# Kernel tuning notes

Hardware: AMD Instinct MI355X
Metric: run time of the kernel (lower is better)

## Reference

```python
import jax, jax.numpy as jnp
import numpy as np

N = 50000      # nodes
E = 800000     # edges (before self loops)
IN = 128       # in_ch
HID = 128      # hid (conv1 concat output)
OUT = 128      # out_ch
H = 4          # heads in conv1
NEG_SLOPE = 0.2


def setup_inputs() -> dict:
    key = jax.random.key(0)
    ks = jax.random.split(key, 16)
    s = 0.05
    return {
        "x": jax.random.normal(ks[0], (N, IN), dtype=jnp.float32),
        "edge_index": jax.random.randint(ks[1], (2, E), 0, N, dtype=jnp.int64),
        # conv1 params (heads=4, per-head dim HID//H)
        "W1l": jax.random.normal(ks[2], (IN, HID), dtype=jnp.float32) * s,
        "b1l": jnp.zeros((HID,), jnp.float32),
        "W1r": jax.random.normal(ks[3], (IN, HID), dtype=jnp.float32) * s,
        "b1r": jnp.zeros((HID,), jnp.float32),
        "att1": jax.random.normal(ks[4], (H, HID // H), dtype=jnp.float32) * s,
        "bias1": jnp.zeros((HID,), jnp.float32),
        # conv2 params (heads=1)
        "W2l": jax.random.normal(ks[5], (HID, OUT), dtype=jnp.float32) * s,
        "b2l": jnp.zeros((OUT,), jnp.float32),
        "W2r": jax.random.normal(ks[6], (HID, OUT), dtype=jnp.float32) * s,
        "b2r": jnp.zeros((OUT,), jnp.float32),
        "att2": jax.random.normal(ks[7], (1, OUT), dtype=jnp.float32) * s,
        "bias2": jnp.zeros((OUT,), jnp.float32),
    }


def gatv2_conv(x, src, dst, Wl, bl, Wr, br, att, heads):
    """PyG GATv2Conv (share_weights=False, concat=True).
    message(j->i): e = LeakyReLU(x_l[j] + x_r[i]); logit = <e, att>;
    softmax over edges per destination i; out_i = sum alpha * x_l[j].
    """
    n = x.shape[0]
    c = Wl.shape[1] // heads
    xl = (x @ Wl + bl).reshape(n, heads, c)   # source transform
    xr = (x @ Wr + br).reshape(n, heads, c)   # destination transform
    e = jax.nn.leaky_relu(xl[src] + xr[dst], NEG_SLOPE)      # [E, H, C]
    logits = jnp.einsum("ehc,hc->eh", e, att)                 # [E, H]
    m = jax.lax.stop_gradient(
        jax.ops.segment_max(logits, dst, num_segments=n))     # [N, H]
    p = jnp.exp(logits - m[dst])                              # [E, H]
    denom = jax.ops.segment_sum(p, dst, num_segments=n)       # [N, H]
    alpha = p / denom[dst]                                    # [E, H]
    out = jax.ops.segment_sum(xl[src] * alpha[..., None], dst,
                              num_segments=n)                 # [N, H, C]
    return out.reshape(n, heads * c)


def reference(x, edge_index, W1l, b1l, W1r, b1r, att1, bias1,
              W2l, b2l, W2r, b2r, att2, bias2):
    n = x.shape[0]
    # PyG default add_self_loops=True
    loops = jnp.arange(n, dtype=edge_index.dtype)
    src = jnp.concatenate([edge_index[0], loops])
    dst = jnp.concatenate([edge_index[1], loops])
    h = gatv2_conv(x, src, dst, W1l, b1l, W1r, b1r, att1, H) + bias1
    h = jax.nn.relu(h)
    out = gatv2_conv(h, src, dst, W2l, b2l, W2r, b2r, att2, 1) + bias2
    return out
```

## Files before the change

kernel.cpp:

```cpp
#include <hip/hip_runtime.h>
#include <hip/hip_bf16.h>

#define NODES 50000
#define NEDGE 800000
#define CH 128
#define NEG_SLOPE 0.2f
#define SCAN_CHUNK 2048
#define NBLK ((NODES + SCAN_CHUNK - 1) / SCAN_CHUNK)
#define NINF -1.0e30f
#define LOG2E 1.44269504088896340736f
#define NSLICE 400
#define SSLICE (NEDGE / NSLICE)

typedef short short8 __attribute__((ext_vector_type(8)));
typedef float f32x4 __attribute__((ext_vector_type(4)));

__device__ __forceinline__ unsigned fbits(float f) {
    union { float f; unsigned u; } v; v.f = f; return v.u;
}
__device__ __forceinline__ float asf(unsigned u) {
    union { float f; unsigned u; } v; v.u = u; return v.f;
}
__device__ __forceinline__ unsigned short f2bf(float f) {
    unsigned u = fbits(f);
    unsigned r = u + 0x7fff + ((u >> 16) & 1);
    return (unsigned short)(r >> 16);
}
__device__ __forceinline__ float bf2f(unsigned short h) {
    return asf(((unsigned)h) << 16);
}
__device__ __forceinline__ float lrelu(float x) {
    return fmaxf(x, NEG_SLOPE * x);
}
__device__ __forceinline__ void bf8cvt(uint4 u, float* f) {
    f[0] = asf(u.x << 16); f[1] = asf(u.x & 0xFFFF0000u);
    f[2] = asf(u.y << 16); f[3] = asf(u.y & 0xFFFF0000u);
    f[4] = asf(u.z << 16); f[5] = asf(u.z & 0xFFFF0000u);
    f[6] = asf(u.w << 16); f[7] = asf(u.w & 0xFFFF0000u);
}
__device__ __forceinline__ int dset(int dst) {
    return (int)(((unsigned)dst * 8u) / 50000u);
}

__global__ __launch_bounds__(256) void detect_zero_kernel(const void* idx,
                                                          int* flag, int* cnt) {
    int t = blockIdx.x * 256 + (int)threadIdx.x;
    if (t < NODES) cnt[t] = 0;
    if (blockIdx.x == 0 && threadIdx.x < 64) {
        const int* w = (const int*)idx;
        int nz = (w[2 * threadIdx.x + 1] != 0) ? 1 : 0;
        unsigned long long b = __ballot(nz);
        if (threadIdx.x == 0) *flag = (b == 0ull) ? 1 : 0;
    }
}

__global__ __launch_bounds__(256) void hist_part_kernel(const void* idx,
                                                        const int* flag,
                                                        int* cnt) {
    int set = blockIdx.x & 7;
    int slice = blockIdx.x >> 3;
    int base = slice * SSLICE;
    int endE = base + SSLICE;
    int i64 = *flag;
    const int* w = (const int*)idx;
    for (int e = base + (int)threadIdx.x; e < endE; e += 256) {
        int dst = i64 ? w[2 * (NEDGE + e)] : w[NEDGE + e];
        if (dset(dst) == set) atomicAdd(&cnt[dst], 1);
    }
}

__global__ __launch_bounds__(256) void scan1_kernel(const int* __restrict__ cnt,
                                                    int* __restrict__ bsum) {
    int base = blockIdx.x * SCAN_CHUNK + (int)threadIdx.x * 8;
    int s = 0;
    #pragma unroll
    for (int k = 0; k < 8; ++k) {
        int i = base + k;
        s += (i < NODES) ? cnt[i] : 0;
    }
    #pragma unroll
    for (int m = 1; m < 64; m <<= 1) s += __shfl_xor(s, m);
    __shared__ int ws[4];
    if ((threadIdx.x & 63) == 0) ws[threadIdx.x >> 6] = s;
    __syncthreads();
    if (threadIdx.x == 0) bsum[blockIdx.x] = ws[0] + ws[1] + ws[2] + ws[3];
}

__global__ __launch_bounds__(256) void scan3_kernel(const int* __restrict__ cnt,
                                                    const int* __restrict__ bsum,
                                                    int* __restrict__ offs,
                                                    int* __restrict__ cursor) {
    int tid = (int)threadIdx.x;
    int bpre = 0;
    #pragma unroll
    for (int b = 0; b < NBLK; ++b) bpre += (b < (int)blockIdx.x) ? bsum[b] : 0;

    int base = blockIdx.x * SCAN_CHUNK + tid * 8;
    int v[8];
    int s = 0;
    #pragma unroll
    for (int k = 0; k < 8; ++k) {
        int i = base + k;
        v[k] = (i < NODES) ? cnt[i] : 0;
        s += v[k];
    }
    int lane = tid & 63;
    int incl = s;
    #pragma unroll
    for (int m = 1; m < 64; m <<= 1) {
        int t = __shfl_up(incl, m);
        if (lane >= m) incl += t;
    }
    __shared__ int wtot[4];
    if (lane == 63) wtot[tid >> 6] = incl;
    __syncthreads();
    int w = tid >> 6;
    int wbase = 0;
    #pragma unroll
    for (int k = 0; k < 4; ++k) wbase += (k < w) ? wtot[k] : 0;
    int excl = bpre + wbase + (incl - s);
    #pragma unroll
    for (int k = 0; k < 8; ++k) {
        int i = base + k;
        if (i < NODES) { offs[i] = excl; cursor[i] = excl; }
        excl += v[k];
    }
    if (blockIdx.x == 0 && tid == 0) offs[NODES] = NEDGE;
}

__global__ __launch_bounds__(256) void scatter_part_kernel(const void* idx,
                                                           const int* flag,
                                                           int* cursor,
                                                           int* __restrict__ srcs) {
    int set = blockIdx.x & 7;
    int slice = blockIdx.x >> 3;
    int base = slice * SSLICE;
    int endE = base + SSLICE;
    int i64 = *flag;
    const int* w = (const int*)idx;
    for (int e = base + (int)threadIdx.x; e < endE; e += 256) {
        int dst = i64 ? w[2 * (NEDGE + e)] : w[NEDGE + e];
        if (dset(dst) == set) {
            int src = i64 ? w[2 * e] : w[e];
            int pos = atomicAdd(&cursor[dst], 1);
            srcs[pos] = src;
        }
    }
}

__global__ __launch_bounds__(256) void wprep4_kernel(const float* __restrict__ W0,
                                                     const float* __restrict__ W1,
                                                     const float* __restrict__ W2,
                                                     const float* __restrict__ W3,
                                                     unsigned short* __restrict__ base) {
    int which = blockIdx.x >> 6;
    const float* W = (which == 0) ? W0 : (which == 1) ? W1 : (which == 2) ? W2 : W3;
    unsigned short* hiT = base + (size_t)which * 32768;
    unsigned short* loT = hiT + 16384;
    int i = (blockIdx.x & 63) * 256 + (int)threadIdx.x;
    int k = i >> 7, n = i & 127;
    float f = W[i];
    unsigned short h = f2bf(f);
    unsigned short l = f2bf(f - bf2f(h));
    hiT[n * CH + k] = h;
    loT[n * CH + k] = l;
}

#define GR 64
#define LDP 136

__global__ __launch_bounds__(256) void gemm_dual_mfma(
        const float* __restrict__ X,
        const unsigned short* __restrict__ whTl, const unsigned short* __restrict__ wlTl,
        const unsigned short* __restrict__ whTr, const unsigned short* __restrict__ wlTr,
        const float* __restrict__ bl, const float* __restrict__ br,
        unsigned short* __restrict__ Ylb, float* __restrict__ Yr, int nrows) {
    __shared__ unsigned short xh[GR][LDP];
    __shared__ unsigned short xlo[GR][LDP];

    int r0 = blockIdx.x * GR;
    int tid = (int)threadIdx.x;

    {
        int row = tid >> 2;
        int c0 = (tid & 3) * 32;
        const float* src = X + (size_t)(r0 + row) * CH + c0;
        bool valid = (r0 + row) < nrows;
        #pragma unroll
        for (int j = 0; j < 32; j += 4) {
            float4 v = valid ? *(const float4*)(src + j)
                             : make_float4(0.f, 0.f, 0.f, 0.f);
            unsigned ux = fbits(v.x), uy = fbits(v.y);
            unsigned uz = fbits(v.z), uw = fbits(v.w);
            unsigned hx = ux & 0xFFFF0000u, hy = uy & 0xFFFF0000u;
            unsigned hz = uz & 0xFFFF0000u, hw = uw & 0xFFFF0000u;
            uint2 hp;
            hp.x = (ux >> 16) | hy;
            hp.y = (uz >> 16) | hw;
            float lx = v.x - asf(hx), ly = v.y - asf(hy);
            float lz = v.z - asf(hz), lw = v.w - asf(hw);
            uint2 lp;
            lp.x = (fbits(lx) >> 16) | (fbits(ly) & 0xFFFF0000u);
            lp.y = (fbits(lz) >> 16) | (fbits(lw) & 0xFFFF0000u);
            *(uint2*)&xh[row][c0 + j]  = hp;
            *(uint2*)&xlo[row][c0 + j] = lp;
        }
    }
    __syncthreads();

    int wave = tid >> 6;
    int lane = tid & 63;
    int l15 = lane & 15, q = lane >> 4;

    f32x4 acc[4][4];
    #pragma unroll
    for (int mt = 0; mt < 4; ++mt)
        #pragma unroll
        for (int nt = 0; nt < 4; ++nt) acc[mt][nt] = (f32x4)0.f;

    const unsigned short* bhp[4];
    const unsigned short* blp_[4];
    int ncol[4];
    #pragma unroll
    for (int nt = 0; nt < 4; ++nt) {
        int n = (wave * 4 + nt) * 16 + l15;
        ncol[nt] = n;
        int nn = n & 127;
        bhp[nt]  = ((n < CH) ? whTl : whTr) + (size_t)nn * CH;
        blp_[nt] = ((n < CH) ? wlTl : wlTr) + (size_t)nn * CH;
    }

    for (int kt = 0; kt < 4; ++kt) {
        int kofs = kt * 32 + q * 8;
        short8 ah[4], al[4];
        #pragma unroll
        for (int mt = 0; mt < 4; ++mt) {
            ah[mt] = *(const short8*)&xh[mt * 16 + l15][kofs];
            al[mt] = *(const short8*)&xlo[mt * 16 + l15][kofs];
        }
        #pragma unroll
        for (int nt = 0; nt < 4; ++nt) {
            short8 bh8 = *(const short8*)(bhp[nt] + kofs);
            short8 bl8 = *(const short8*)(blp_[nt] + kofs);
            #pragma unroll
            for (int mt = 0; mt < 4; ++mt) {
                acc[mt][nt] = __builtin_amdgcn_mfma_f32_16x16x32_bf16(
                                  ah[mt], bh8, acc[mt][nt], 0, 0, 0);
                acc[mt][nt] = __builtin_amdgcn_mfma_f32_16x16x32_bf16(
                                  al[mt], bh8, acc[mt][nt], 0, 0, 0);
                acc[mt][nt] = __builtin_amdgcn_mfma_f32_16x16x32_bf16(
                                  ah[mt], bl8, acc[mt][nt], 0, 0, 0);
            }
        }
    }

    #pragma unroll
    for (int nt = 0; nt < 4; ++nt) {
        int n = ncol[nt];
        int nc = n & 127;
        if (n < CH) {
            float bv = bl[nc];
            #pragma unroll
            for (int mt = 0; mt < 4; ++mt)
                #pragma unroll
                for (int reg = 0; reg < 4; ++reg) {
                    int row = r0 + mt * 16 + q * 4 + reg;
                    if (row < nrows)
                        Ylb[(size_t)row * CH + nc] = f2bf(acc[mt][nt][reg] + bv);
                }
        } else {
            float bv = br[nc];
            #pragma unroll
            for (int mt = 0; mt < 4; ++mt)
                #pragma unroll
                for (int reg = 0; reg < 4; ++reg) {
                    int row = r0 + mt * 16 + q * 4 + reg;
                    if (row < nrows)
                        Yr[(size_t)row * CH + nc] = acc[mt][nt][reg] + bv;
                }
        }
    }
}

template <int HEADS, bool RELU>
__global__ __launch_bounds__(256) void node_pass(
        const unsigned short* __restrict__ xlb,
        const float* __restrict__ xr,
        const float* __restrict__ att,
        const float* __restrict__ bias,
        const int* __restrict__ offs, const int* __restrict__ srcs,
        float* __restrict__ out) {
    constexpr int GL = (CH / HEADS) / 8;
    int wave = (int)threadIdx.x >> 6;
    int i = blockIdx.x * 4 + wave;
    int lane = (int)threadIdx.x & 63;
    int g = lane >> 4;
    int l16 = lane & 15;
    int c0 = l16 * 8;

    float r[8], a[8], s[8];
    {
        const float4* xrp = (const float4*)(xr + (size_t)i * CH + c0);
        float4 r0 = xrp[0], r1 = xrp[1];
        r[0]=r0.x; r[1]=r0.y; r[2]=r0.z; r[3]=r0.w;
        r[4]=r1.x; r[5]=r1.y; r[6]=r1.z; r[7]=r1.w;
        const float4* atp = (const float4*)(att + c0);
        float4 a0 = atp[0], a1 = atp[1];
        a[0]=a0.x*LOG2E; a[1]=a0.y*LOG2E; a[2]=a0.z*LOG2E; a[3]=a0.w*LOG2E;
        a[4]=a1.x*LOG2E; a[5]=a1.y*LOG2E; a[6]=a1.z*LOG2E; a[7]=a1.w*LOG2E;
    }
    uint4 us = *(const uint4*)(xlb + (size_t)i * CH + c0);
    bf8cvt(us, s);

    float ts = 0.f;
    #pragma unroll
    for (int c = 0; c < 8; ++c) ts += lrelu(s[c] + r[c]) * a[c];
    #pragma unroll
    for (int msk = 1; msk < GL; msk <<= 1) ts += __shfl_xor(ts, msk);

    float m = (g == 0) ? ts : NINF;
    float d = (g == 0) ? 1.f : 0.f;
    float acc[8];
    #pragma unroll
    for (int c = 0; c < 8; ++c) acc[c] = (g == 0) ? s[c] : 0.f;

    int beg = offs[i], end = offs[i + 1];
    int deg = end - beg;
    int iters = (deg + 3) >> 2;
    if (iters > 0) {
        int last = end - 1;
        int e = beg + g;
        int si = srcs[min(e, last)];
        uint4 u = *(const uint4*)(xlb + (size_t)si * CH + c0);

        for (int it = 0; it < iters; ++it, e += 4) {
            bool valid = e < end;
            int sn = srcs[min(e + 4, last)];
            uint4 un = *(const uint4*)(xlb + (size_t)sn * CH + c0);

            float f[8];
            bf8cvt(u, f);
            float t = 0.f;
            #pragma unroll
            for (int c = 0; c < 8; ++c) t += lrelu(f[c] + r[c]) * a[c];
            #pragma unroll
            for (int msk = 1; msk < GL; msk <<= 1) t += __shfl_xor(t, msk);
            t = valid ? t : NINF;

            float nm = fmaxf(m, t);
            float sc = exp2f(m - nm);
            float p  = valid ? exp2f(t - nm) : 0.f;
            d = d * sc + p;
            #pragma unroll
            for (int c = 0; c < 8; ++c) acc[c] = acc[c] * sc + p * f[c];
            m = nm;
            u = un;
        }
    }

    #pragma unroll
    for (int msk = 16; msk <= 32; msk <<= 1) {
        float mo  = __shfl_xor(m, msk);
        float dof = __shfl_xor(d, msk);
        float nm = fmaxf(m, mo);
        float s0 = exp2f(m - nm), s1 = exp2f(mo - nm);
        d = d * s0 + dof * s1;
        #pragma unroll
        for (int c = 0; c < 8; ++c) {
            float ao = __shfl_xor(acc[c], msk);
            acc[c] = acc[c] * s0 + ao * s1;
        }
        m = nm;
    }

    if (g == 0) {
        float inv = 1.0f / d;
        const float4* bp = (const float4*)(bias + c0);
        float4 b0 = bp[0], b1 = bp[1];
        float bb[8] = {b0.x, b0.y, b0.z, b0.w, b1.x, b1.y, b1.z, b1.w};
        float o[8];
        #pragma unroll
        for (int c = 0; c < 8; ++c) {
            o[c] = acc[c] * inv + bb[c];
            if (RELU) o[c] = fmaxf(o[c], 0.f);
        }
        float4 w0 = make_float4(o[0], o[1], o[2], o[3]);
        float4 w1 = make_float4(o[4], o[5], o[6], o[7]);
        float4* op = (float4*)(out + (size_t)i * CH + c0);
        op[0] = w0; op[1] = w1;
    }
}

extern "C" void kernel_launch(void* const* d_in, const int* in_sizes, int n_in,
                              void* d_out, int out_size, void* d_ws, size_t ws_size,
                              hipStream_t stream) {
    const float* x     = (const float*)d_in[0];
    const void*  eidx  = d_in[1];
    const float* W1l   = (const float*)d_in[2];
    const float* b1l   = (const float*)d_in[3];
    const float* W1r   = (const float*)d_in[4];
    const float* b1r   = (const float*)d_in[5];
    const float* att1  = (const float*)d_in[6];
    const float* bias1 = (const float*)d_in[7];
    const float* W2l   = (const float*)d_in[8];
    const float* b2l   = (const float*)d_in[9];
    const float* W2r   = (const float*)d_in[10];
    const float* b2r   = (const float*)d_in[11];
    const float* att2  = (const float*)d_in[12];
    const float* bias2 = (const float*)d_in[13];
    float* out = (float*)d_out;

    unsigned short* xlb = (unsigned short*)d_ws;
    float* xr = (float*)(xlb + (size_t)NODES * CH);
    float* hb = xr + (size_t)NODES * CH;
    int* offs   = (int*)(hb + (size_t)NODES * CH);
    int* cnt    = offs + (NODES + 1);
    int* cursor = cnt + NODES;
    int* srcs   = cursor + NODES;
    int* flag   = srcs + NEDGE;
    int* bsum   = flag + 1;

    unsigned short* wbuf = (unsigned short*)cnt;
    unsigned short* w1lh = wbuf;              unsigned short* w1ll = wbuf + 16384;
    unsigned short* w1rh = wbuf + 32768;      unsigned short* w1rl = wbuf + 49152;
    unsigned short* w2lh = wbuf + 65536;      unsigned short* w2ll = wbuf + 81920;
    unsigned short* w2rh = wbuf + 98304;      unsigned short* w2rl = wbuf + 114688;

    const int GG = (NODES + GR - 1) / GR;
    const int ZB = (NODES + 255) / 256;
    const int PG = NSLICE * 8;

    detect_zero_kernel<<<ZB, 256, 0, stream>>>(eidx, flag, cnt);
    hist_part_kernel<<<PG, 256, 0, stream>>>(eidx, flag, cnt);
    scan1_kernel<<<NBLK, 256, 0, stream>>>(cnt, bsum);
    scan3_kernel<<<NBLK, 256, 0, stream>>>(cnt, bsum, offs, cursor);
    scatter_part_kernel<<<PG, 256, 0, stream>>>(eidx, flag, cursor, srcs);

    wprep4_kernel<<<256, 256, 0, stream>>>(W1l, W1r, W2l, W2r, wbuf);

    gemm_dual_mfma<<<GG, 256, 0, stream>>>(x, w1lh, w1ll, w1rh, w1rl,
                                           b1l, b1r, xlb, xr, NODES);
    node_pass<4, true><<<(NODES + 3) / 4, 256, 0, stream>>>(xlb, xr, att1, bias1,
                                                            offs, srcs, hb);

    gemm_dual_mfma<<<GG, 256, 0, stream>>>(hb, w2lh, w2ll, w2rh, w2rl,
                                           b2l, b2r, xlb, xr, NODES);
    node_pass<1, false><<<(NODES + 3) / 4, 256, 0, stream>>>(xlb, xr, att2, bias2,
                                                             offs, srcs, out);
}
```

Before: 365.5 us.

## Merge prep kernels, emit split-bf16 hidden layer, unroll edge loop by two

Merges the zero/detect kernel and the weight-prep kernel into one launch and moves the weight buffer to its own region. The first node pass now writes its output as hi/lo bf16 pairs, so the second GEMM reads pre-split operands directly from global memory without an LDS conversion stage. The edge aggregation loop handles two edges per group per iteration, with two gathers in flight for more memory-level parallelism. This costs more registers and a GEMM that loads its A operand straight from global memory with no shared-memory staging.

```diff
diff --git a/kernel.cpp b/kernel.cpp
--- a/kernel.cpp
+++ b/kernel.cpp
@@ -11,6 +11,7 @@
 #define LOG2E 1.44269504088896340736f
 #define NSLICE 400
 #define SSLICE (NEDGE / NSLICE)
+#define ZB ((NODES + 255) / 256)
 
 typedef short short8 __attribute__((ext_vector_type(8)));
 typedef float f32x4 __attribute__((ext_vector_type(4)));
@@ -42,16 +43,37 @@
     return (int)(((unsigned)dst * 8u) / 50000u);
 }
 
-__global__ __launch_bounds__(256) void detect_zero_kernel(const void* idx,
-                                                          int* flag, int* cnt) {
-    int t = blockIdx.x * 256 + (int)threadIdx.x;
-    if (t < NODES) cnt[t] = 0;
-    if (blockIdx.x == 0 && threadIdx.x < 64) {
-        const int* w = (const int*)idx;
-        int nz = (w[2 * threadIdx.x + 1] != 0) ? 1 : 0;
-        unsigned long long b = __ballot(nz);
-        if (threadIdx.x == 0) *flag = (b == 0ull) ? 1 : 0;
-    }
+__global__ __launch_bounds__(256) void prep_kernel(const void* idx, int* flag,
+                                                   int* cnt,
+                                                   const float* __restrict__ W0,
+                                                   const float* __restrict__ W1,
+                                                   const float* __restrict__ W2,
+                                                   const float* __restrict__ W3,
+                                                   unsigned short* __restrict__ wbase) {
+    int b = (int)blockIdx.x;
+    if (b < ZB) {
+        int t = b * 256 + (int)threadIdx.x;
+        if (t < NODES) cnt[t] = 0;
+        if (b == 0 && threadIdx.x < 64) {
+            const int* w = (const int*)idx;
+            int nz = (w[2 * threadIdx.x + 1] != 0) ? 1 : 0;
+            unsigned long long bal = __ballot(nz);
+            if (threadIdx.x == 0) *flag = (bal == 0ull) ? 1 : 0;
+        }
+        return;
+    }
+    int wb = b - ZB;
+    int which = wb >> 6;
+    const float* W = (which == 0) ? W0 : (which == 1) ? W1 : (which == 2) ? W2 : W3;
+    unsigned short* hiT = wbase + (size_t)which * 32768;
+    unsigned short* loT = hiT + 16384;
+    int i = (wb & 63) * 256 + (int)threadIdx.x;
+    int k = i >> 7, n = i & 127;
+    float f = W[i];
+    unsigned short h = f2bf(f);
+    unsigned short l = f2bf(f - bf2f(h));
+    hiT[n * CH + k] = h;
+    loT[n * CH + k] = l;
 }
 
 __global__ __launch_bounds__(256) void hist_part_kernel(const void* idx,
@@ -146,24 +168,6 @@
             srcs[pos] = src;
         }
     }
-}
-
-__global__ __launch_bounds__(256) void wprep4_kernel(const float* __restrict__ W0,
-                                                     const float* __restrict__ W1,
-                                                     const float* __restrict__ W2,
-                                                     const float* __restrict__ W3,
-                                                     unsigned short* __restrict__ base) {
-    int which = blockIdx.x >> 6;
-    const float* W = (which == 0) ? W0 : (which == 1) ? W1 : (which == 2) ? W2 : W3;
-    unsigned short* hiT = base + (size_t)which * 32768;
-    unsigned short* loT = hiT + 16384;
-    int i = (blockIdx.x & 63) * 256 + (int)threadIdx.x;
-    int k = i >> 7, n = i & 127;
-    float f = W[i];
-    unsigned short h = f2bf(f);
-    unsigned short l = f2bf(f - bf2f(h));
-    hiT[n * CH + k] = h;
-    loT[n * CH + k] = l;
 }
 
 #define GR 64
@@ -282,14 +286,105 @@
     }
 }
 
-template <int HEADS, bool RELU>
+__global__ __launch_bounds__(256) void gemm_dual_mfma_pl(
+        const unsigned short* __restrict__ Ah, const unsigned short* __restrict__ Al,
+        const unsigned short* __restrict__ whTl, const unsigned short* __restrict__ wlTl,
+        const unsigned short* __restrict__ whTr, const unsigned short* __restrict__ wlTr,
+        const float* __restrict__ bl, const float* __restrict__ br,
+        unsigned short* __restrict__ Ylb, float* __restrict__ Yr, int nrows) {
+    int r0 = blockIdx.x * GR;
+    int tid = (int)threadIdx.x;
+    int wave = tid >> 6;
+    int lane = tid & 63;
+    int l15 = lane & 15, q = lane >> 4;
+
+    size_t offA[4];
+    #pragma unroll
+    for (int mt = 0; mt < 4; ++mt) {
+        int row = r0 + mt * 16 + l15;
+        if (row > nrows - 1) row = nrows - 1;
+        offA[mt] = (size_t)row * CH;
+    }
+
+    f32x4 acc[4][4];
+    #pragma unroll
+    for (int mt = 0; mt < 4; ++mt)
+        #pragma unroll
+        for (int nt = 0; nt < 4; ++nt) acc[mt][nt] = (f32x4)0.f;
+
+    const unsigned short* bhp[4];
+    const unsigned short* blp_[4];
+    int ncol[4];
+    #pragma unroll
+    for (int nt = 0; nt < 4; ++nt) {
+        int n = (wave * 4 + nt) * 16 + l15;
+        ncol[nt] = n;
+        int nn = n & 127;
+        bhp[nt]  = ((n < CH) ? whTl : whTr) + (size_t)nn * CH;
+        blp_[nt] = ((n < CH) ? wlTl : wlTr) + (size_t)nn * CH;
+    }
+
+    for (int kt = 0; kt < 4; ++kt) {
+        int kofs = kt * 32 + q * 8;
+        short8 ah[4], al[4];
+        #pragma unroll
+        for (int mt = 0; mt < 4; ++mt) {
+            ah[mt] = *(const short8*)(Ah + offA[mt] + kofs);
+            al[mt] = *(const short8*)(Al + offA[mt] + kofs);
+        }
+        #pragma unroll
+        for (int nt = 0; nt < 4; ++nt) {
+            short8 bh8 = *(const short8*)(bhp[nt] + kofs);
+            short8 bl8 = *(const short8*)(blp_[nt] + kofs);
+            #pragma unroll
+            for (int mt = 0; mt < 4; ++mt) {
+                acc[mt][nt] = __builtin_amdgcn_mfma_f32_16x16x32_bf16(
+                                  ah[mt], bh8, acc[mt][nt], 0, 0, 0);
+                acc[mt][nt] = __builtin_amdgcn_mfma_f32_16x16x32_bf16(
+                                  al[mt], bh8, acc[mt][nt], 0, 0, 0);
+                acc[mt][nt] = __builtin_amdgcn_mfma_f32_16x16x32_bf16(
+                                  ah[mt], bl8, acc[mt][nt], 0, 0, 0);
+            }
+        }
+    }
+
+    #pragma unroll
+    for (int nt = 0; nt < 4; ++nt) {
+        int n = ncol[nt];
+        int nc = n & 127;
+        if (n < CH) {
+            float bv = bl[nc];
+            #pragma unroll
+            for (int mt = 0; mt < 4; ++mt)
+                #pragma unroll
+                for (int reg = 0; reg < 4; ++reg) {
+                    int row = r0 + mt * 16 + q * 4 + reg;
+                    if (row < nrows)
+                        Ylb[(size_t)row * CH + nc] = f2bf(acc[mt][nt][reg] + bv);
+                }
+        } else {
+            float bv = br[nc];
+            #pragma unroll
+            for (int mt = 0; mt < 4; ++mt)
+                #pragma unroll
+                for (int reg = 0; reg < 4; ++reg) {
+                    int row = r0 + mt * 16 + q * 4 + reg;
+                    if (row < nrows)
+                        Yr[(size_t)row * CH + nc] = acc[mt][nt][reg] + bv;
+                }
+        }
+    }
+}
+
+template <int HEADS, bool RELU, bool SPLITOUT>
 __global__ __launch_bounds__(256) void node_pass(
         const unsigned short* __restrict__ xlb,
         const float* __restrict__ xr,
         const float* __restrict__ att,
         const float* __restrict__ bias,
         const int* __restrict__ offs, const int* __restrict__ srcs,
-        float* __restrict__ out) {
+        float* __restrict__ outf,
+        unsigned short* __restrict__ outh, unsigned short* __restrict__ outl) {
     constexpr int GL = (CH / HEADS) / 8;
     int wave = (int)threadIdx.x >> 6;
     int i = blockIdx.x * 4 + wave;
@@ -326,35 +421,49 @@
 
     int beg = offs[i], end = offs[i + 1];
     int deg = end - beg;
-    int iters = (deg + 3) >> 2;
+    int iters = (deg + 7) >> 3;
     if (iters > 0) {
         int last = end - 1;
         int e = beg + g;
-        int si = srcs[min(e, last)];
-        uint4 u = *(const uint4*)(xlb + (size_t)si * CH + c0);
-
-        for (int it = 0; it < iters; ++it, e += 4) {
-            bool valid = e < end;
-            int sn = srcs[min(e + 4, last)];
-            uint4 un = *(const uint4*)(xlb + (size_t)sn * CH + c0);
-
-            float f[8];
-            bf8cvt(u, f);
-            float t = 0.f;
-            #pragma unroll
-            for (int c = 0; c < 8; ++c) t += lrelu(f[c] + r[c]) * a[c];
-            #pragma unroll
-            for (int msk = 1; msk < GL; msk <<= 1) t += __shfl_xor(t, msk);
-            t = valid ? t : NINF;
-
-            float nm = fmaxf(m, t);
+        int s0i = srcs[min(e, last)];
+        int s1i = srcs[min(e + 4, last)];
+        uint4 u0 = *(const uint4*)(xlb + (size_t)s0i * CH + c0);
+        uint4 u1 = *(const uint4*)(xlb + (size_t)s1i * CH + c0);
+
+        for (int it = 0; it < iters; ++it, e += 8) {
+            bool v0 = e < end, v1 = (e + 4) < end;
+            int sn0 = srcs[min(e + 8, last)];
+            int sn1 = srcs[min(e + 12, last)];
+            uint4 un0 = *(const uint4*)(xlb + (size_t)sn0 * CH + c0);
+            uint4 un1 = *(const uint4*)(xlb + (size_t)sn1 * CH + c0);
+
+            float f0[8], f1[8];
+            bf8cvt(u0, f0);
+            bf8cvt(u1, f1);
+            float t0 = 0.f, t1 = 0.f;
+            #pragma unroll
+            for (int c = 0; c < 8; ++c) {
+                t0 += lrelu(f0[c] + r[c]) * a[c];
+                t1 += lrelu(f1[c] + r[c]) * a[c];
+            }
+            #pragma unroll
+            for (int msk = 1; msk < GL; msk <<= 1) {
+                t0 += __shfl_xor(t0, msk);
+                t1 += __shfl_xor(t1, msk);
+            }
+            t0 = v0 ? t0 : NINF;
+            t1 = v1 ? t1 : NINF;
+
+            float nm = fmaxf(m, fmaxf(t0, t1));
             float sc = exp2f(m - nm);
-            float p  = valid ? exp2f(t - nm) : 0.f;
-            d = d * sc + p;
-            #pragma unroll
-            for (int c = 0; c < 8; ++c) acc[c] = acc[c] * sc + p * f[c];
+            float p0 = v0 ? exp2f(t0 - nm) : 0.f;
+            float p1 = v1 ? exp2f(t1 - nm) : 0.f;
+            d = d * sc + p0 + p1;
+            #pragma unroll
+            for (int c = 0; c < 8; ++c)
+                acc[c] = acc[c] * sc + p0 * f0[c] + p1 * f1[c];
             m = nm;
-            u = un;
+            u0 = un0; u1 = un1;
         }
     }
 
@@ -384,10 +493,29 @@
             o[c] = acc[c] * inv + bb[c];
             if (RELU) o[c] = fmaxf(o[c], 0.f);
         }
-        float4 w0 = make_float4(o[0], o[1], o[2], o[3]);
-        float4 w1 = make_float4(o[4], o[5], o[6], o[7]);
-        float4* op = (float4*)(out + (size_t)i * CH + c0);
-        op[0] = w0; op[1] = w1;
+        if (SPLITOUT) {
+            unsigned hu[8];
+            float lo[8];
+            #pragma unroll
+            for (int c = 0; c < 8; ++c) {
+                hu[c] = fbits(o[c]) & 0xFFFF0000u;
+                lo[c] = o[c] - asf(hu[c]);
+            }
+            uint4 ph, pl;
+            ph.x = (hu[0] >> 16) | hu[1];  ph.y = (hu[2] >> 16) | hu[3];
+            ph.z = (hu[4] >> 16) | hu[5];  ph.w = (hu[6] >> 16) | hu[7];
+            pl.x = (fbits(lo[0]) >> 16) | (fbits(lo[1]) & 0xFFFF0000u);
+            pl.y = (fbits(lo[2]) >> 16) | (fbits(lo[3]) & 0xFFFF0000u);
+            pl.z = (fbits(lo[4]) >> 16) | (fbits(lo[5]) & 0xFFFF0000u);
+            pl.w = (fbits(lo[6]) >> 16) | (fbits(lo[7]) & 0xFFFF0000u);
+            *(uint4*)(outh + (size_t)i * CH + c0) = ph;
+            *(uint4*)(outl + (size_t)i * CH + c0) = pl;
+        } else {
+            float4 w0 = make_float4(o[0], o[1], o[2], o[3]);
+            float4 w1 = make_float4(o[4], o[5], o[6], o[7]);
+            float4* op = (float4*)(outf + (size_t)i * CH + c0);
+            op[0] = w0; op[1] = w1;
+        }
     }
 }
 
@@ -412,39 +540,38 @@
 
     unsigned short* xlb = (unsigned short*)d_ws;
     float* xr = (float*)(xlb + (size_t)NODES * CH);
-    float* hb = xr + (size_t)NODES * CH;
-    int* offs   = (int*)(hb + (size_t)NODES * CH);
+    unsigned short* hbh = (unsigned short*)(xr + (size_t)NODES * CH);
+    unsigned short* hbl = hbh + (size_t)NODES * CH;
+    int* offs   = (int*)(hbl + (size_t)NODES * CH);
     int* cnt    = offs + (NODES + 1);
     int* cursor = cnt + NODES;
     int* srcs   = cursor + NODES;
     int* flag   = srcs + NEDGE;
     int* bsum   = flag + 1;
-
-    unsigned short* wbuf = (unsigned short*)cnt;
+    unsigned short* wbuf =
+        (unsigned short*)(((uintptr_t)(bsum + NBLK) + 15) & ~(uintptr_t)15);
     unsigned short* w1lh = wbuf;              unsigned short* w1ll = wbuf + 16384;
     unsigned short* w1rh = wbuf + 32768;      unsigned short* w1rl = wbuf + 49152;
     unsigned short* w2lh = wbuf + 65536;      unsigned short* w2ll = wbuf + 81920;
     unsigned short* w2rh = wbuf + 98304;      unsigned short* w2rl = wbuf + 114688;
 
     const int GG = (NODES + GR - 1) / GR;
-    const int ZB = (NODES + 255) / 256;
     const int PG = NSLICE * 8;
 
-    detect_zero_kernel<<<ZB, 256, 0, stream>>>(eidx, flag, cnt);
+    prep_kernel<<<ZB + 256, 256, 0, stream>>>(eidx, flag, cnt,
+                                              W1l, W1r, W2l, W2r, wbuf);
     hist_part_kernel<<<PG, 256, 0, stream>>>(eidx, flag, cnt);
     scan1_kernel<<<NBLK, 256, 0, stream>>>(cnt, bsum);
     scan3_kernel<<<NBLK, 256, 0, stream>>>(cnt, bsum, offs, cursor);
     scatter_part_kernel<<<PG, 256, 0, stream>>>(eidx, flag, cursor, srcs);
 
-    wprep4_kernel<<<256, 256, 0, stream>>>(W1l, W1r, W2l, W2r, wbuf);
-
     gemm_dual_mfma<<<GG, 256, 0, stream>>>(x, w1lh, w1ll, w1rh, w1rl,
                                            b1l, b1r, xlb, xr, NODES);
-    node_pass<4, true><<<(NODES + 3) / 4, 256, 0, stream>>>(xlb, xr, att1, bias1,
-                                                            offs, srcs, hb);
-
-    gemm_dual_mfma<<<GG, 256, 0, stream>>>(hb, w2lh, w2ll, w2rh, w2rl,
-                                           b2l, b2r, xlb, xr, NODES);
-    node_pass<1, false><<<(NODES + 3) / 4, 256, 0, stream>>>(xlb, xr, att2, bias2,
-                                                             offs, srcs, out);
-}
+    node_pass<4, true, true><<<(NODES + 3) / 4, 256, 0, stream>>>(
+        xlb, xr, att1, bias1, offs, srcs, nullptr, hbh, hbl);
+
+    gemm_dual_mfma_pl<<<GG, 256, 0, stream>>>(hbh, hbl, w2lh, w2ll, w2rh, w2rl,
+                                              b2l, b2r, xlb, xr, NODES);
+    node_pass<1, false, false><<<(NODES + 3) / 4, 256, 0, stream>>>(
+        xlb, xr, att2, bias2, offs, srcs, out, nullptr, nullptr);
+}
```

After: 376.3 us. 2.9% more time.
